# Performance work log

Measured on AMD Instinct MI355X. Metric: run time of the kernel, lower is better.

The kernel has to match this reference:

```python
import jax, jax.numpy as jnp
import numpy as np

TEMPERATURE = 0.1
NUM_CLASSES = 4  # matches fill_max of labels
NEG_INF = -1e9
EPS = 1e-6


def setup_inputs() -> dict:
    key = jax.random.key(0)
    k1, k2 = jax.random.split(key)
    emb = jax.random.normal(k1, (2, 128, 64, 64), dtype=jnp.float32)
    labels = jax.random.randint(k2, (2, 64, 64), 0, NUM_CLASSES, dtype=jnp.int32)
    return {"emb": emb, "labels": labels}


def reference(emb, labels):
    B, C, H, W = emb.shape
    e = emb.transpose(0, 2, 3, 1).reshape(B * H * W, C)      # [N, C]
    lab = labels.reshape(B * H * W)                           # [N]
    # F.normalize(dim=1) with eps clamp
    norm = jnp.maximum(jnp.linalg.norm(e, axis=1, keepdims=True), 1e-12)
    e = e / norm
    n = e.shape[0]
    logits = (e @ e.T) / TEMPERATURE                          # [N, N]
    diag = jnp.arange(n)
    logits = logits.at[diag, diag].set(NEG_INF)               # mask self
    ex = jnp.exp(logits)                                      # [N, N]
    same = lab[:, None] == lab[None, :]                       # [N, N] bool
    pos_sum = jnp.sum(jnp.where(same, ex, 0.0), axis=1)       # [N]
    tot_sum = jnp.sum(ex, axis=1)                             # [N]
    row_loss = -jnp.log(pos_sum / (tot_sum + EPS))            # [N]
    # per-class mean, averaged over classes present (== torch.unique loop)
    sums = jax.ops.segment_sum(row_loss, lab, num_segments=NUM_CLASSES)
    counts = jax.ops.segment_sum(jnp.ones_like(row_loss), lab, num_segments=NUM_CLASSES)
    present = counts > 0
    per_cls = jnp.where(present, sums / jnp.maximum(counts, 1.0), 0.0)
    return per_cls.sum() / present.sum()
```

## Files before the change

### kernel.cpp

```cpp
#include <hip/hip_runtime.h>
#include <hip/hip_bf16.h>

#define N_PIX 8192
#define C_DIM 128
#define HW 4096
#define PRESCALE 3.7982825f
#define NUM_CLASSES 4

typedef __attribute__((ext_vector_type(8))) short short8;
typedef __attribute__((ext_vector_type(4))) float float4v;


__global__ __launch_bounds__(256) void normscale_kernel(const float* __restrict__ emb,
                                                        unsigned short* __restrict__ ebfT,
                                                        float* __restrict__ pz) {
    const int tid = threadIdx.x;
    const int p16 = tid & 15;
    const int g = tid >> 4;
    const int n = blockIdx.x * 16 + p16;
    const int b = n >> 12;
    const int hw = n & (HW - 1);
    const float* base = emb + b * (C_DIM * HW) + hw;

    float v[8];
    float ss = 0.f;
#pragma unroll
    for (int i = 0; i < 8; ++i) {
        v[i] = base[(g * 8 + i) * HW];
        ss += v[i] * v[i];
    }
    ss += __shfl_xor(ss, 16, 64);
    ss += __shfl_xor(ss, 32, 64);
    __shared__ float red[4][16];
    const int wv = tid >> 6;
    if ((tid & 63) < 16) red[wv][p16] = ss;
    __syncthreads();
    float tot = red[0][p16] + red[1][p16] + red[2][p16] + red[3][p16];
    float inv = PRESCALE / fmaxf(sqrtf(tot), 1e-12f);

    unsigned short us[8];
#pragma unroll
    for (int i = 0; i < 8; ++i) {
        __hip_bfloat16 h = __float2bfloat16(v[i] * inv);
        us[i] = *reinterpret_cast<unsigned short*>(&h);
    }
    const int s = g >> 2, quad = g & 3;
    unsigned short* dst = ebfT + (((blockIdx.x * 4 + s) * 64 + quad * 16 + p16) << 3);
    *reinterpret_cast<short8*>(dst) = *reinterpret_cast<short8*>(us);

    if (blockIdx.x < 64) pz[blockIdx.x * 256 + tid] = 0.f;
}

__global__ __launch_bounds__(256, 4) void pairwise_kernel(const unsigned short* __restrict__ ebfT,
                                                          const int* __restrict__ lab,
                                                          float* __restrict__ pos,
                                                          float* __restrict__ tot) {
    const int bi = blockIdx.x;
    const int d = blockIdx.y + 1;
    if (d == 32 && bi >= 32) return;
    const int jp = (bi + d) & 63;
    const int Ipanel = bi << 7;
    const int Jpanel = jp << 7;

    const int wave = threadIdx.x >> 6;
    const int lane = threadIdx.x & 63;
    const int quad = lane >> 4;
    const int lq = lane & 15;

    const int I0 = Ipanel + wave * 32;

    short8 afrag[2][4];
#pragma unroll
    for (int a = 0; a < 2; ++a) {
        const unsigned short* ab = ebfT + ((((I0 >> 4) + a) * 4) * 64 + lane) * 8;
#pragma unroll
        for (int s = 0; s < 4; ++s)
            afrag[a][s] = *reinterpret_cast<const short8*>(ab + s * 512);
    }
    int lab_row[2][4];
#pragma unroll
    for (int a = 0; a < 2; ++a)
#pragma unroll
        for (int r = 0; r < 4; ++r) lab_row[a][r] = lab[I0 + a * 16 + quad * 4 + r];

    float tacc[2][4] = {};
    float pacc[2][4] = {};

    {
        const unsigned short* bbase = ebfT + ((Jpanel >> 4) * 4 * 64 + lane) * 8;
        for (int t = 0; t < 8; ++t) {
            const int lab_col = lab[Jpanel + t * 16 + lq];
            const unsigned short* bt = bbase + t * 2048;
            short8 bfrag[4];
#pragma unroll
            for (int s = 0; s < 4; ++s)
                bfrag[s] = *reinterpret_cast<const short8*>(bt + s * 512);

            float4v acc0 = {0.f, 0.f, 0.f, 0.f};
            float4v acc1 = {0.f, 0.f, 0.f, 0.f};
#pragma unroll
            for (int s = 0; s < 4; ++s) {
                acc0 = __builtin_amdgcn_mfma_f32_16x16x32_bf16(afrag[0][s], bfrag[s], acc0, 0, 0, 0);
                acc1 = __builtin_amdgcn_mfma_f32_16x16x32_bf16(afrag[1][s], bfrag[s], acc1, 0, 0, 0);
            }

            float colTs = 0.f, colPs = 0.f;
#pragma unroll
            for (int r = 0; r < 4; ++r) {
                float ex = __builtin_amdgcn_exp2f(acc0[r]);
                tacc[0][r] += ex;
                float pxe = (lab_row[0][r] == lab_col) ? ex : 0.f;
                pacc[0][r] += pxe;
                colTs += ex;
                colPs += pxe;
            }
#pragma unroll
            for (int r = 0; r < 4; ++r) {
                float ex = __builtin_amdgcn_exp2f(acc1[r]);
                tacc[1][r] += ex;
                float pxe = (lab_row[1][r] == lab_col) ? ex : 0.f;
                pacc[1][r] += pxe;
                colTs += ex;
                colPs += pxe;
            }
            colTs += __shfl_xor(colTs, 16, 64);
            colTs += __shfl_xor(colTs, 32, 64);
            colPs += __shfl_xor(colPs, 16, 64);
            colPs += __shfl_xor(colPs, 32, 64);
            if (quad == 0) {
                atomicAdd(&tot[Jpanel + t * 16 + lq], colTs);
                atomicAdd(&pos[Jpanel + t * 16 + lq], colPs);
            }
        }
    }

#define EPILOGUE(A, ACC, MASKED)                                            \
    {                                                                       \
        _Pragma("unroll") for (int r = 0; r < 4; ++r) {                     \
            float ex = __builtin_amdgcn_exp2f(ACC[r]);                      \
            if (MASKED) ex = (lq == quad * 4 + r) ? 0.f : ex;               \
            tacc[A][r] += ex;                                               \
            pacc[A][r] += (lab_row[A][r] == lab_col) ? ex : 0.f;            \
        }                                                                   \
    }
    if (d == 1) {
        const unsigned short* bbase = ebfT + ((Ipanel >> 4) * 4 * 64 + lane) * 8;
        for (int t = 0; t < 8; ++t) {
            const int J = Ipanel + t * 16;
            const int lab_col = lab[J + lq];
            const unsigned short* bt = bbase + t * 2048;
            short8 bfrag[4];
#pragma unroll
            for (int s = 0; s < 4; ++s)
                bfrag[s] = *reinterpret_cast<const short8*>(bt + s * 512);

            float4v acc0 = {0.f, 0.f, 0.f, 0.f};
            float4v acc1 = {0.f, 0.f, 0.f, 0.f};
#pragma unroll
            for (int s = 0; s < 4; ++s) {
                acc0 = __builtin_amdgcn_mfma_f32_16x16x32_bf16(afrag[0][s], bfrag[s], acc0, 0, 0, 0);
                acc1 = __builtin_amdgcn_mfma_f32_16x16x32_bf16(afrag[1][s], bfrag[s], acc1, 0, 0, 0);
            }
            if (J == I0) EPILOGUE(0, acc0, true) else EPILOGUE(0, acc0, false);
            if (J == I0 + 16) EPILOGUE(1, acc1, true) else EPILOGUE(1, acc1, false);
        }
    }
#undef EPILOGUE

#pragma unroll
    for (int a = 0; a < 2; ++a) {
#pragma unroll
        for (int r = 0; r < 4; ++r) {
            float t = tacc[a][r], p = pacc[a][r];
#pragma unroll
            for (int off = 1; off < 16; off <<= 1) {
                t += __shfl_xor(t, off, 64);
                p += __shfl_xor(p, off, 64);
            }
            if (lq == 0) {
                const int row = I0 + a * 16 + quad * 4 + r;
                atomicAdd(&tot[row], t);
                atomicAdd(&pos[row], p);
            }
        }
    }
}

__global__ __launch_bounds__(1024) void finalize_kernel(const float* __restrict__ pos,
                                                        const float* __restrict__ tot,
                                                        const int* __restrict__ lab,
                                                        float* __restrict__ out) {
    const int tid = threadIdx.x;
    float ls[NUM_CLASSES] = {0.f, 0.f, 0.f, 0.f};
    float lc[NUM_CLASSES] = {0.f, 0.f, 0.f, 0.f};
#pragma unroll
    for (int it = 0; it < N_PIX / 1024; ++it) {
        const int n = it * 1024 + tid;
        float rl = logf(tot[n] + 1e-6f) - logf(pos[n]);
        int c = lab[n];
#pragma unroll
        for (int k = 0; k < NUM_CLASSES; ++k) {
            if (c == k) {
                ls[k] += rl;
                lc[k] += 1.f;
            }
        }
    }
#pragma unroll
    for (int off = 1; off < 64; off <<= 1) {
#pragma unroll
        for (int k = 0; k < NUM_CLASSES; ++k) {
            ls[k] += __shfl_xor(ls[k], off, 64);
            lc[k] += __shfl_xor(lc[k], off, 64);
        }
    }
    __shared__ float ssum[16][NUM_CLASSES];
    __shared__ float scnt[16][NUM_CLASSES];
    const int wid = tid >> 6;
    if ((tid & 63) == 0) {
#pragma unroll
        for (int k = 0; k < NUM_CLASSES; ++k) {
            ssum[wid][k] = ls[k];
            scnt[wid][k] = lc[k];
        }
    }
    __syncthreads();
    if (tid == 0) {
        float acc = 0.f;
        int present = 0;
        for (int k = 0; k < NUM_CLASSES; ++k) {
            float s = 0.f, c = 0.f;
            for (int w = 0; w < 16; ++w) {
                s += ssum[w][k];
                c += scnt[w][k];
            }
            if (c > 0.f) {
                acc += s / c;
                present++;
            }
        }
        out[0] = acc / (float)(present > 0 ? present : 1);
    }
}

extern "C" void kernel_launch(void* const* d_in, const int* in_sizes, int n_in,
                              void* d_out, int out_size, void* d_ws, size_t ws_size,
                              hipStream_t stream) {
    const float* emb = (const float*)d_in[0];
    const int* lab = (const int*)d_in[1];
    float* out = (float*)d_out;

    unsigned short* ebfT = (unsigned short*)d_ws;
    float* pos = (float*)((char*)d_ws + N_PIX * C_DIM * 2);
    float* tot = pos + N_PIX;

    normscale_kernel<<<N_PIX / 16, 256, 0, stream>>>(emb, ebfT, pos);

    dim3 grid(64, 32);
    pairwise_kernel<<<grid, 256, 0, stream>>>(ebfT, lab, pos, tot);

    finalize_kernel<<<1, 1024, 0, stream>>>(pos, tot, lab, out);
}
```

Baseline: 95.26 us.

## Batch column-sum atomics through shared memory and unroll the tile loop

Per-tile column sums are now kept in registers across the unrolled 8-tile loop instead of being reduced and atomically added every iteration. After the loop, each wave reduces its column sums across quads, writes them to shared memory, and one block-level pass issues a single atomic per column for tot and pos. This removes the per-iteration cross-lane shuffles and three quarters of the global atomic traffic (one atomic per column per block instead of one per wave). The cost is extra registers and a __syncthreads, which could affect occupancy.

```diff
diff --git a/kernel.cpp b/kernel.cpp
--- a/kernel.cpp
+++ b/kernel.cpp
@@ -85,9 +85,12 @@
 
     float tacc[2][4] = {};
     float pacc[2][4] = {};
+    float colT_r[8] = {};
+    float colP_r[8] = {};
 
     {
         const unsigned short* bbase = ebfT + ((Jpanel >> 4) * 4 * 64 + lane) * 8;
+#pragma unroll
         for (int t = 0; t < 8; ++t) {
             const int lab_col = lab[Jpanel + t * 16 + lq];
             const unsigned short* bt = bbase + t * 2048;
@@ -104,15 +107,14 @@
                 acc1 = __builtin_amdgcn_mfma_f32_16x16x32_bf16(afrag[1][s], bfrag[s], acc1, 0, 0, 0);
             }
 
-            float colTs = 0.f, colPs = 0.f;
 #pragma unroll
             for (int r = 0; r < 4; ++r) {
                 float ex = __builtin_amdgcn_exp2f(acc0[r]);
                 tacc[0][r] += ex;
                 float pxe = (lab_row[0][r] == lab_col) ? ex : 0.f;
                 pacc[0][r] += pxe;
-                colTs += ex;
-                colPs += pxe;
+                colT_r[t] += ex;
+                colP_r[t] += pxe;
             }
 #pragma unroll
             for (int r = 0; r < 4; ++r) {
@@ -120,16 +122,8 @@
                 tacc[1][r] += ex;
                 float pxe = (lab_row[1][r] == lab_col) ? ex : 0.f;
                 pacc[1][r] += pxe;
-                colTs += ex;
-                colPs += pxe;
-            }
-            colTs += __shfl_xor(colTs, 16, 64);
-            colTs += __shfl_xor(colTs, 32, 64);
-            colPs += __shfl_xor(colPs, 16, 64);
-            colPs += __shfl_xor(colPs, 32, 64);
-            if (quad == 0) {
-                atomicAdd(&tot[Jpanel + t * 16 + lq], colTs);
-                atomicAdd(&pos[Jpanel + t * 16 + lq], colPs);
+                colT_r[t] += ex;
+                colP_r[t] += pxe;
             }
         }
     }
@@ -184,6 +178,29 @@
             }
         }
     }
+
+    __shared__ float clsT[4][128];
+    __shared__ float clsP[4][128];
+#pragma unroll
+    for (int t = 0; t < 8; ++t) {
+        float ct = colT_r[t], cp = colP_r[t];
+        ct += __shfl_xor(ct, 16, 64);
+        ct += __shfl_xor(ct, 32, 64);
+        cp += __shfl_xor(cp, 16, 64);
+        cp += __shfl_xor(cp, 32, 64);
+        if (quad == 0) {
+            clsT[wave][t * 16 + lq] = ct;
+            clsP[wave][t * 16 + lq] = cp;
+        }
+    }
+    __syncthreads();
+    if (threadIdx.x < 128) {
+        const int c = threadIdx.x;
+        atomicAdd(&tot[Jpanel + c], clsT[0][c] + clsT[1][c] + clsT[2][c] + clsT[3][c]);
+    } else {
+        const int c = threadIdx.x - 128;
+        atomicAdd(&pos[Jpanel + c], clsP[0][c] + clsP[1][c] + clsP[2][c] + clsP[3][c]);
+    }
 }
 
 __global__ __launch_bounds__(1024) void finalize_kernel(const float* __restrict__ pos,
```

Result: slower. 176.5 us (+85.3%).
